# Kernel tuning notes

Measured on AMD Instinct MI355X. Metric: run time of the kernel, lower is better.

## Reference

```python
import jax, jax.numpy as jnp
import numpy as np

N = 50000
E = 1600000
IN_DIM = 128
HEADS = 4
OUT_DIM = 32
NEG_SLOPE = 0.2


def setup_inputs() -> dict:
    key = jax.random.key(0)
    k1, k2, k3, k4, k5, k6 = jax.random.split(key, 6)
    x = jax.random.normal(k1, (N, IN_DIM), dtype=jnp.float32)
    src = jax.random.randint(k2, (E,), 0, N)
    dst = jax.random.randint(k3, (E,), 0, N)
    edge_index = jnp.stack([src, dst], axis=0).astype(jnp.int64)
    W = jax.random.normal(k4, (IN_DIM, HEADS * OUT_DIM), dtype=jnp.float32) * 0.08
    att = jax.random.normal(k5, (HEADS, 2 * OUT_DIM), dtype=jnp.float32) * 0.1
    bias = jnp.zeros((HEADS * OUT_DIM,), dtype=jnp.float32)
    return {"x": x, "edge_index": edge_index, "W": W, "att": att, "bias": bias}


def reference(x, edge_index, W, att, bias):
    src, dst = edge_index[0], edge_index[1]
    n = x.shape[0]
    # Linear projection -> [N, H, F]
    Wh = (x @ W).reshape(n, HEADS, OUT_DIM)
    # Per-node attention score halves (equivalent to (cat[Wh_i,Wh_j]*att).sum(-1))
    a_src = jnp.einsum("nhf,hf->nh", Wh, att[:, :OUT_DIM])  # [N, H]
    a_dst = jnp.einsum("nhf,hf->nh", Wh, att[:, OUT_DIM:])  # [N, H]
    logits = jax.nn.leaky_relu(a_src[src] + a_dst[dst], negative_slope=NEG_SLOPE)  # [E, H]
    # Segment softmax over destination nodes (numerically stable)
    seg_max = jax.ops.segment_max(logits, dst, num_segments=n)  # [N, H]
    exp_s = jnp.exp(logits - seg_max[dst])
    denom = jnp.clip(jax.ops.segment_sum(exp_s, dst, num_segments=n), 1e-9, None)
    alpha = exp_s / denom[dst]  # [E, H]
    # Weighted messages from SOURCE features, scatter-sum to destinations
    messages = alpha[:, :, None] * Wh[src]  # [E, H, F]
    out = jax.ops.segment_sum(messages.reshape(-1, HEADS * OUT_DIM), dst, num_segments=n)
    return out + bias
```

## Files before the change

kernel.cpp:

```cpp
#include <hip/hip_runtime.h>
#include <hip/hip_fp16.h>
#include <math.h>

#define N_NODES 50000
#define E_EDGES 1600000
#define IN_DIM 128
#define HEADS 4
#define OUT_DIM 32
#define HF 128
#define NEG_SLOPE 0.2f
#define NBUCK 196
#define BCAP 8800

typedef _Float16 half8 __attribute__((ext_vector_type(8)));
typedef float float4v __attribute__((ext_vector_type(4)));

__global__ __launch_bounds__(256) void gat_wt(
        const float* __restrict__ W, _Float16* __restrict__ Wt) {
    const int n = blockIdx.x * 2 + (threadIdx.x >> 7);
    const int k = threadIdx.x & 127;
    Wt[n * 128 + k] = (_Float16)W[k * 128 + n];
}

__global__ __launch_bounds__(256) void gat_proj(
        const float* __restrict__ x, const _Float16* __restrict__ Wt,
        const float* __restrict__ att, __half* __restrict__ Whh,
        float* __restrict__ a_src, float* __restrict__ a_dst) {
    __shared__ _Float16 xsh[64][136];
    __shared__ float4 wfrag[2048 / 4 * 8 / 8];
    __shared__ float atts[256];

    const int tid  = threadIdx.x;
    const int lane = tid & 63;
    const int wv   = tid >> 6;
    const int l15  = lane & 15;
    const int quad = lane >> 4;

    if (tid < 64) ((float4*)atts)[tid] = ((const float4*)att)[tid];

    const int rowBase  = blockIdx.x * 64;
    const int rowsHere = min(64, N_NODES - rowBase);

    const float4* x4 = (const float4*)(x + (size_t)rowBase * IN_DIM);
    for (int i = tid; i < rowsHere * 32; i += 256) {
        const int r = i >> 5, q = i & 31;
        float4 v = x4[i];
        _Float16* p = &xsh[r][q * 4];
        p[0] = (_Float16)v.x; p[1] = (_Float16)v.y;
        p[2] = (_Float16)v.z; p[3] = (_Float16)v.w;
    }

    __shared__ float4 wf[32 * 64];
    for (int i = tid; i < 32 * 64; i += 256) {
        const int ln = i & 63, c = i >> 6;
        const int s = c >> 3, t = c & 7;
        const int n = t * 16 + (ln & 15);
        const int k = s * 32 + (ln >> 4) * 8;
        wf[i] = *(const float4*)(Wt + n * 128 + k);
    }
    __syncthreads();

    float4v acc[8] = {};
    half8 afr[4];
#pragma unroll
    for (int s = 0; s < 4; ++s)
        afr[s] = *(const half8*)&xsh[wv * 16 + l15][s * 32 + quad * 8];
#pragma unroll
    for (int s = 0; s < 4; ++s) {
#pragma unroll
        for (int t = 0; t < 8; ++t) {
            half8 b = *(const half8*)&wf[(s * 8 + t) * 64 + lane];
            acc[t] = __builtin_amdgcn_mfma_f32_16x16x32_f16(afr[s], b, acc[t], 0, 0, 0);
        }
    }

    float ps[4][4] = {}, pd[4][4] = {};
#pragma unroll
    for (int t = 0; t < 8; ++t) {
        const int g = t >> 1;
        const int f = ((t & 1) << 4) + l15;
        const float as_ = atts[g * 64 + f];
        const float ad_ = atts[g * 64 + 32 + f];
#pragma unroll
        for (int reg = 0; reg < 4; ++reg) {
            ps[reg][g] = fmaf(acc[t][reg], as_, ps[reg][g]);
            pd[reg][g] = fmaf(acc[t][reg], ad_, pd[reg][g]);
        }
    }
#pragma unroll
    for (int reg = 0; reg < 4; ++reg) {
        const int rloc = wv * 16 + quad * 4 + reg;
        const int row = rowBase + rloc;
        if (rloc < rowsHere) {
#pragma unroll
            for (int t = 0; t < 8; ++t)
                Whh[(size_t)row * HF + t * 16 + l15] = __float2half(acc[t][reg]);
        }
#pragma unroll
        for (int g = 0; g < 4; ++g) {
#pragma unroll
            for (int d = 1; d < 16; d <<= 1) {
                ps[reg][g] += __shfl_xor(ps[reg][g], d, 64);
                pd[reg][g] += __shfl_xor(pd[reg][g], d, 64);
            }
        }
        if (rloc < rowsHere && l15 < 4) {
            a_src[row * HEADS + l15] = ps[reg][l15];
            a_dst[row * HEADS + l15] = pd[reg][l15];
        }
    }
}

__global__ __launch_bounds__(256) void gat_p1(
        const int* __restrict__ ei, int* __restrict__ gCount,
        unsigned int* __restrict__ gBuck) {
    __shared__ int hist[NBUCK];
    __shared__ int cur[NBUCK];
    const int t = threadIdx.x;
    for (int i = t; i < NBUCK; i += 256) hist[i] = 0;
    __syncthreads();

    unsigned int keys[16];
    bool valid[4];
    const int base4 = blockIdx.x * 1024 + t;
#pragma unroll
    for (int j = 0; j < 4; ++j) {
        const int i4 = base4 + 256 * j;
        valid[j] = (i4 < E_EDGES / 4);
        if (valid[j]) {
            const int4 s4 = ((const int4*)ei)[i4];
            const int4 d4 = ((const int4*)(ei + E_EDGES))[i4];
            keys[j * 4 + 0] = ((unsigned)d4.x << 16) | (unsigned)s4.x;
            keys[j * 4 + 1] = ((unsigned)d4.y << 16) | (unsigned)s4.y;
            keys[j * 4 + 2] = ((unsigned)d4.z << 16) | (unsigned)s4.z;
            keys[j * 4 + 3] = ((unsigned)d4.w << 16) | (unsigned)s4.w;
#pragma unroll
            for (int q = 0; q < 4; ++q)
                atomicAdd(&hist[keys[j * 4 + q] >> 24], 1);
        }
    }
    __syncthreads();
    for (int i = t; i < NBUCK; i += 256)
        cur[i] = atomicAdd(&gCount[i], hist[i]);
    __syncthreads();
#pragma unroll
    for (int j = 0; j < 4; ++j) {
        if (!valid[j]) continue;
#pragma unroll
        for (int q = 0; q < 4; ++q) {
            const unsigned int k = keys[j * 4 + q];
            const int b = k >> 24;
            const int p = atomicAdd(&cur[b], 1);
            if (p < BCAP) gBuck[(size_t)b * BCAP + p] = k;
        }
    }
}

__global__ __launch_bounds__(256) void gat_p2(
        const int* __restrict__ gCount, const unsigned int* __restrict__ gBuck,
        unsigned short* __restrict__ csr, int* __restrict__ offsets) {
    __shared__ int pre[256];
    __shared__ int hist[256];
    __shared__ int loc[256];
    __shared__ unsigned short out16[BCAP];
    const int b = blockIdx.x;
    const int t = threadIdx.x;

    int v = (t < NBUCK) ? min(gCount[t], BCAP) : 0;
    pre[t] = v;
    __syncthreads();
#pragma unroll
    for (int d = 1; d < 256; d <<= 1) {
        int u = (t >= d) ? pre[t - d] : 0;
        __syncthreads();
        pre[t] += u;
        __syncthreads();
    }
    const int total = pre[255];
    const int baseb = (b > 0) ? pre[b - 1] : 0;
    const int cnt = min(gCount[b], BCAP);

    hist[t] = 0;
    __syncthreads();
    for (int i = t; i < cnt; i += 256)
        atomicAdd(&hist[(gBuck[(size_t)b * BCAP + i] >> 16) & 255], 1);
    __syncthreads();
    const int hv = hist[t];
    loc[t] = hv;
    __syncthreads();
#pragma unroll
    for (int d = 1; d < 256; d <<= 1) {
        int u = (t >= d) ? loc[t - d] : 0;
        __syncthreads();
        loc[t] += u;
        __syncthreads();
    }
    const int myloc = loc[t] - hv;
    const int node = b * 256 + t;
    if (node < N_NODES) offsets[node] = baseb + myloc;
    if (b == 0 && t == 0) offsets[N_NODES] = total;
    __syncthreads();

    hist[t] = myloc;
    __syncthreads();
    for (int i = t; i < cnt; i += 256) {
        const unsigned int k = gBuck[(size_t)b * BCAP + i];
        const int n = (k >> 16) & 255;
        const int r = atomicAdd(&hist[n], 1);
        out16[r] = (unsigned short)(k & 0xFFFFu);
    }
    __syncthreads();
    for (int i = t; i < cnt; i += 256)
        csr[baseb + i] = out16[i];
}

__global__ __launch_bounds__(256) void gat_gather(
        const int* __restrict__ offsets, const unsigned short* __restrict__ csr,
        const float* __restrict__ a_src, const float* __restrict__ a_dst,
        const __half* __restrict__ Whh, const float* __restrict__ bias,
        float* __restrict__ out) {
    const int node = blockIdx.x * 4 + (threadIdx.x >> 6);
    const int lane = threadIdx.x & 63;
    if (node >= N_NODES) return;
    const int h = lane >> 4;
    const int hbase = lane & 48;
    const int sub = lane & 15;
    const float ad = a_dst[node * HEADS + h];
    const __half2* __restrict__ Wh2 = (const __half2*)Whh;

    float accx = 0.f, accy = 0.f, denOwn = 0.f;
    const int beg = offsets[node];
    const int cnt = offsets[node + 1] - beg;

    for (int base = 0; base < cnt; base += 64) {
        const int rem = min(64, cnt - base);
        const int idx = (base + lane < cnt) ? (int)csr[beg + base + lane] : 0;
        const int nchunk = (rem + 15) >> 4;
        for (int cj = 0; cj < nchunk; ++cj) {
            const int e0 = cj << 4;
            const int sOwn = __shfl(idx, e0 + sub, 64);
            float t = a_src[sOwn * 4 + h] + ad;
            t = fmaxf(t, NEG_SLOPE * t);
            float wOwn = __expf(t);
            if (base + e0 + sub >= cnt) wOwn = 0.f;
            denOwn += wOwn;

            const int jmax = min(16, rem - e0);
            if (jmax == 16) {
                int ss[16];
#pragma unroll
                for (int j = 0; j < 16; ++j) ss[j] = __shfl(idx, e0 + j, 64);
                __half2 vv[16];
#pragma unroll
                for (int j = 0; j < 16; ++j)
                    vv[j] = Wh2[(size_t)ss[j] * 64 + lane];
                float ww[16];
#pragma unroll
                for (int j = 0; j < 16; ++j) ww[j] = __shfl(wOwn, hbase + j, 64);
#pragma unroll
                for (int j = 0; j < 16; ++j) {
                    const float2 f = __half22float2(vv[j]);
                    accx = fmaf(ww[j], f.x, accx);
                    accy = fmaf(ww[j], f.y, accy);
                }
            } else {
                for (int j = 0; j < jmax; ++j) {
                    const int s = __shfl(idx, e0 + j, 64);
                    const float w = __shfl(wOwn, hbase + j, 64);
                    const float2 v = __half22float2(Wh2[(size_t)s * 64 + lane]);
                    accx = fmaf(w, v.x, accx);
                    accy = fmaf(w, v.y, accy);
                }
            }
        }
    }
    float den = denOwn;
    den += __shfl_xor(den, 1, 64);
    den += __shfl_xor(den, 2, 64);
    den += __shfl_xor(den, 4, 64);
    den += __shfl_xor(den, 8, 64);

    const float inv = 1.f / fmaxf(den, 1e-9f);
    const float2 b2 = ((const float2*)bias)[lane];
    float2 o = {accx * inv + b2.x, accy * inv + b2.y};
    ((float2*)out)[(size_t)node * 64 + lane] = o;
}

extern "C" void kernel_launch(void* const* d_in, const int* in_sizes, int n_in,
                              void* d_out, int out_size, void* d_ws, size_t ws_size,
                              hipStream_t stream) {
    const float* x    = (const float*)d_in[0];
    const int*   ei   = (const int*)d_in[1];
    const float* W    = (const float*)d_in[2];
    const float* att  = (const float*)d_in[3];
    const float* bias = (const float*)d_in[4];
    float* out = (float*)d_out;

    __half* Whh   = (__half*)d_ws;
    float* a_src  = (float*)(Whh + (size_t)N_NODES * HF);
    float* a_dst  = a_src + (size_t)N_NODES * HEADS;
    unsigned int* gBuck = (unsigned int*)(a_dst + (size_t)N_NODES * HEADS);
    unsigned short* csr = (unsigned short*)(gBuck + (size_t)NBUCK * BCAP);
    int*   offsets = (int*)(csr + (size_t)E_EDGES);
    int*   gCount  = offsets + N_NODES + 8;
    _Float16* Wt   = (_Float16*)(gCount + 256);

    hipMemsetAsync(gCount, 0, NBUCK * sizeof(int), stream);
    gat_wt<<<64, 256, 0, stream>>>(W, Wt);
    gat_proj<<<(N_NODES + 63) / 64, 256, 0, stream>>>(x, Wt, att, Whh, a_src, a_dst);
    gat_p1<<<(E_EDGES / 4 + 1023) / 1024, 256, 0, stream>>>(ei, gCount, gBuck);
    gat_p2<<<NBUCK, 256, 0, stream>>>(gCount, gBuck, csr, offsets);
    gat_gather<<<(N_NODES + 3) / 4, 256, 0, stream>>>(offsets, csr, a_src,
                                                      a_dst, Whh, bias, out);
}
```

Measured before the change: 211.2 us.

## Fuse projection and edge bucketing into one launch; fold memset into prep

The memset of the bucket counters moves into the W-transpose kernel. The projection and edge-bucketing kernels become a single launch that splits blocks by index, so the two independent stages can run concurrently and two launches are dropped. The gather inner loop replaces the fully unrolled 16-edge path with a 4-way unrolled loop plus a remainder loop. This lowers register pressure but keeps fewer loads in flight. The fused kernel uses a 51 KB shared buffer for all blocks, which may reduce occupancy for the bucketing blocks.

Result: faster. 186.8 us (-11.6%).

```diff
diff --git a/kernel.cpp b/kernel.cpp
--- a/kernel.cpp
+++ b/kernel.cpp
@@ -11,147 +11,151 @@
 #define NEG_SLOPE 0.2f
 #define NBUCK 196
 #define BCAP 8800
+#define PROJ_NB 782
+#define P1_NB 391
 
 typedef _Float16 half8 __attribute__((ext_vector_type(8)));
 typedef float float4v __attribute__((ext_vector_type(4)));
 
-__global__ __launch_bounds__(256) void gat_wt(
-        const float* __restrict__ W, _Float16* __restrict__ Wt) {
+__global__ __launch_bounds__(256) void gat_prep(
+        const float* __restrict__ W, _Float16* __restrict__ Wt,
+        int* __restrict__ gCount) {
+    if (blockIdx.x == 0 && threadIdx.x < NBUCK) gCount[threadIdx.x] = 0;
     const int n = blockIdx.x * 2 + (threadIdx.x >> 7);
     const int k = threadIdx.x & 127;
     Wt[n * 128 + k] = (_Float16)W[k * 128 + n];
 }
 
-__global__ __launch_bounds__(256) void gat_proj(
+__global__ __launch_bounds__(256) void gat_fused(
         const float* __restrict__ x, const _Float16* __restrict__ Wt,
         const float* __restrict__ att, __half* __restrict__ Whh,
-        float* __restrict__ a_src, float* __restrict__ a_dst) {
-    __shared__ _Float16 xsh[64][136];
-    __shared__ float4 wfrag[2048 / 4 * 8 / 8];
-    __shared__ float atts[256];
-
-    const int tid  = threadIdx.x;
-    const int lane = tid & 63;
-    const int wv   = tid >> 6;
-    const int l15  = lane & 15;
-    const int quad = lane >> 4;
-
-    if (tid < 64) ((float4*)atts)[tid] = ((const float4*)att)[tid];
-
-    const int rowBase  = blockIdx.x * 64;
-    const int rowsHere = min(64, N_NODES - rowBase);
-
-    const float4* x4 = (const float4*)(x + (size_t)rowBase * IN_DIM);
-    for (int i = tid; i < rowsHere * 32; i += 256) {
-        const int r = i >> 5, q = i & 31;
-        float4 v = x4[i];
-        _Float16* p = &xsh[r][q * 4];
-        p[0] = (_Float16)v.x; p[1] = (_Float16)v.y;
-        p[2] = (_Float16)v.z; p[3] = (_Float16)v.w;
-    }
-
-    __shared__ float4 wf[32 * 64];
-    for (int i = tid; i < 32 * 64; i += 256) {
-        const int ln = i & 63, c = i >> 6;
-        const int s = c >> 3, t = c & 7;
-        const int n = t * 16 + (ln & 15);
-        const int k = s * 32 + (ln >> 4) * 8;
-        wf[i] = *(const float4*)(Wt + n * 128 + k);
-    }
-    __syncthreads();
-
-    float4v acc[8] = {};
-    half8 afr[4];
-#pragma unroll
-    for (int s = 0; s < 4; ++s)
-        afr[s] = *(const half8*)&xsh[wv * 16 + l15][s * 32 + quad * 8];
-#pragma unroll
-    for (int s = 0; s < 4; ++s) {
-#pragma unroll
-        for (int t = 0; t < 8; ++t) {
-            half8 b = *(const half8*)&wf[(s * 8 + t) * 64 + lane];
-            acc[t] = __builtin_amdgcn_mfma_f32_16x16x32_f16(afr[s], b, acc[t], 0, 0, 0);
-        }
-    }
-
-    float ps[4][4] = {}, pd[4][4] = {};
-#pragma unroll
-    for (int t = 0; t < 8; ++t) {
-        const int g = t >> 1;
-        const int f = ((t & 1) << 4) + l15;
-        const float as_ = atts[g * 64 + f];
-        const float ad_ = atts[g * 64 + 32 + f];
-#pragma unroll
-        for (int reg = 0; reg < 4; ++reg) {
-            ps[reg][g] = fmaf(acc[t][reg], as_, ps[reg][g]);
-            pd[reg][g] = fmaf(acc[t][reg], ad_, pd[reg][g]);
-        }
-    }
-#pragma unroll
-    for (int reg = 0; reg < 4; ++reg) {
-        const int rloc = wv * 16 + quad * 4 + reg;
-        const int row = rowBase + rloc;
-        if (rloc < rowsHere) {
-#pragma unroll
-            for (int t = 0; t < 8; ++t)
-                Whh[(size_t)row * HF + t * 16 + l15] = __float2half(acc[t][reg]);
-        }
-#pragma unroll
-        for (int g = 0; g < 4; ++g) {
-#pragma unroll
-            for (int d = 1; d < 16; d <<= 1) {
-                ps[reg][g] += __shfl_xor(ps[reg][g], d, 64);
-                pd[reg][g] += __shfl_xor(pd[reg][g], d, 64);
-            }
-        }
-        if (rloc < rowsHere && l15 < 4) {
-            a_src[row * HEADS + l15] = ps[reg][l15];
-            a_dst[row * HEADS + l15] = pd[reg][l15];
-        }
-    }
-}
-
-__global__ __launch_bounds__(256) void gat_p1(
+        float* __restrict__ a_src, float* __restrict__ a_dst,
         const int* __restrict__ ei, int* __restrict__ gCount,
         unsigned int* __restrict__ gBuck) {
-    __shared__ int hist[NBUCK];
-    __shared__ int cur[NBUCK];
-    const int t = threadIdx.x;
-    for (int i = t; i < NBUCK; i += 256) hist[i] = 0;
-    __syncthreads();
-
-    unsigned int keys[16];
-    bool valid[4];
-    const int base4 = blockIdx.x * 1024 + t;
-#pragma unroll
-    for (int j = 0; j < 4; ++j) {
-        const int i4 = base4 + 256 * j;
-        valid[j] = (i4 < E_EDGES / 4);
-        if (valid[j]) {
-            const int4 s4 = ((const int4*)ei)[i4];
-            const int4 d4 = ((const int4*)(ei + E_EDGES))[i4];
-            keys[j * 4 + 0] = ((unsigned)d4.x << 16) | (unsigned)s4.x;
-            keys[j * 4 + 1] = ((unsigned)d4.y << 16) | (unsigned)s4.y;
-            keys[j * 4 + 2] = ((unsigned)d4.z << 16) | (unsigned)s4.z;
-            keys[j * 4 + 3] = ((unsigned)d4.w << 16) | (unsigned)s4.w;
-#pragma unroll
-            for (int q = 0; q < 4; ++q)
-                atomicAdd(&hist[keys[j * 4 + q] >> 24], 1);
-        }
-    }
-    __syncthreads();
-    for (int i = t; i < NBUCK; i += 256)
-        cur[i] = atomicAdd(&gCount[i], hist[i]);
-    __syncthreads();
-#pragma unroll
-    for (int j = 0; j < 4; ++j) {
-        if (!valid[j]) continue;
-#pragma unroll
-        for (int q = 0; q < 4; ++q) {
-            const unsigned int k = keys[j * 4 + q];
-            const int b = k >> 24;
-            const int p = atomicAdd(&cur[b], 1);
-            if (p < BCAP) gBuck[(size_t)b * BCAP + p] = k;
+    __shared__ __align__(16) char smem[51200];
+    const int tid = threadIdx.x;
+
+    if (blockIdx.x < PROJ_NB) {
+        _Float16 (*xsh)[136] = (_Float16(*)[136])smem;
+        float4* wf  = (float4*)(smem + 17408);
+        float* atts = (float*)(smem + 17408 + 32768);
+
+        const int lane = tid & 63;
+        const int wv   = tid >> 6;
+        const int l15  = lane & 15;
+        const int quad = lane >> 4;
+
+        if (tid < 64) ((float4*)atts)[tid] = ((const float4*)att)[tid];
+
+        const int rowBase  = blockIdx.x * 64;
+        const int rowsHere = min(64, N_NODES - rowBase);
+
+        const float4* x4 = (const float4*)(x + (size_t)rowBase * IN_DIM);
+        for (int i = tid; i < rowsHere * 32; i += 256) {
+            const int r = i >> 5, q = i & 31;
+            float4 v = x4[i];
+            _Float16* p = &xsh[r][q * 4];
+            p[0] = (_Float16)v.x; p[1] = (_Float16)v.y;
+            p[2] = (_Float16)v.z; p[3] = (_Float16)v.w;
+        }
+        for (int i = tid; i < 32 * 64; i += 256) {
+            const int ln = i & 63, c = i >> 6;
+            const int s = c >> 3, t = c & 7;
+            const int n = t * 16 + (ln & 15);
+            const int k = s * 32 + (ln >> 4) * 8;
+            wf[i] = *(const float4*)(Wt + n * 128 + k);
+        }
+        __syncthreads();
+
+        float4v acc[8] = {};
+        half8 afr[4];
+#pragma unroll
+        for (int s = 0; s < 4; ++s)
+            afr[s] = *(const half8*)&xsh[wv * 16 + l15][s * 32 + quad * 8];
+#pragma unroll
+        for (int s = 0; s < 4; ++s) {
+#pragma unroll
+            for (int t = 0; t < 8; ++t) {
+                half8 b = *(const half8*)&wf[(s * 8 + t) * 64 + lane];
+                acc[t] = __builtin_amdgcn_mfma_f32_16x16x32_f16(afr[s], b, acc[t], 0, 0, 0);
+            }
+        }
+
+        float ps[4][4] = {}, pd[4][4] = {};
+#pragma unroll
+        for (int t = 0; t < 8; ++t) {
+            const int g = t >> 1;
+            const int f = ((t & 1) << 4) + l15;
+            const float as_ = atts[g * 64 + f];
+            const float ad_ = atts[g * 64 + 32 + f];
+#pragma unroll
+            for (int reg = 0; reg < 4; ++reg) {
+                ps[reg][g] = fmaf(acc[t][reg], as_, ps[reg][g]);
+                pd[reg][g] = fmaf(acc[t][reg], ad_, pd[reg][g]);
+            }
+        }
+#pragma unroll
+        for (int reg = 0; reg < 4; ++reg) {
+            const int rloc = wv * 16 + quad * 4 + reg;
+            const int row = rowBase + rloc;
+            if (rloc < rowsHere) {
+#pragma unroll
+                for (int t = 0; t < 8; ++t)
+                    Whh[(size_t)row * HF + t * 16 + l15] = __float2half(acc[t][reg]);
+            }
+#pragma unroll
+            for (int g = 0; g < 4; ++g) {
+#pragma unroll
+                for (int d = 1; d < 16; d <<= 1) {
+                    ps[reg][g] += __shfl_xor(ps[reg][g], d, 64);
+                    pd[reg][g] += __shfl_xor(pd[reg][g], d, 64);
+                }
+            }
+            if (rloc < rowsHere && l15 < 4) {
+                a_src[row * HEADS + l15] = ps[reg][l15];
+                a_dst[row * HEADS + l15] = pd[reg][l15];
+            }
+        }
+    } else {
+        int* hist = (int*)smem;
+        int* cur  = hist + NBUCK;
+        const int bid = blockIdx.x - PROJ_NB;
+        for (int i = tid; i < NBUCK; i += 256) hist[i] = 0;
+        __syncthreads();
+
+        unsigned int keys[16];
+        bool valid[4];
+        const int base4 = bid * 1024 + tid;
+#pragma unroll
+        for (int j = 0; j < 4; ++j) {
+            const int i4 = base4 + 256 * j;
+            valid[j] = (i4 < E_EDGES / 4);
+            if (valid[j]) {
+                const int4 s4 = ((const int4*)ei)[i4];
+                const int4 d4 = ((const int4*)(ei + E_EDGES))[i4];
+                keys[j * 4 + 0] = ((unsigned)d4.x << 16) | (unsigned)s4.x;
+                keys[j * 4 + 1] = ((unsigned)d4.y << 16) | (unsigned)s4.y;
+                keys[j * 4 + 2] = ((unsigned)d4.z << 16) | (unsigned)s4.z;
+                keys[j * 4 + 3] = ((unsigned)d4.w << 16) | (unsigned)s4.w;
+#pragma unroll
+                for (int q = 0; q < 4; ++q)
+                    atomicAdd(&hist[keys[j * 4 + q] >> 24], 1);
+            }
+        }
+        __syncthreads();
+        for (int i = tid; i < NBUCK; i += 256)
+            cur[i] = atomicAdd(&gCount[i], hist[i]);
+        __syncthreads();
+#pragma unroll
+        for (int j = 0; j < 4; ++j) {
+            if (!valid[j]) continue;
+#pragma unroll
+            for (int q = 0; q < 4; ++q) {
+                const unsigned int k = keys[j * 4 + q];
+                const int b = k >> 24;
+                const int p = atomicAdd(&cur[b], 1);
+                if (p < BCAP) gBuck[(size_t)b * BCAP + p] = k;
+            }
         }
     }
 }
@@ -246,31 +250,35 @@
             denOwn += wOwn;
 
             const int jmax = min(16, rem - e0);
-            if (jmax == 16) {
-                int ss[16];
-#pragma unroll
-                for (int j = 0; j < 16; ++j) ss[j] = __shfl(idx, e0 + j, 64);
-                __half2 vv[16];
-#pragma unroll
-                for (int j = 0; j < 16; ++j)
-                    vv[j] = Wh2[(size_t)ss[j] * 64 + lane];
-                float ww[16];
-#pragma unroll
-                for (int j = 0; j < 16; ++j) ww[j] = __shfl(wOwn, hbase + j, 64);
-#pragma unroll
-                for (int j = 0; j < 16; ++j) {
-                    const float2 f = __half22float2(vv[j]);
-                    accx = fmaf(ww[j], f.x, accx);
-                    accy = fmaf(ww[j], f.y, accy);
-                }
-            } else {
-                for (int j = 0; j < jmax; ++j) {
-                    const int s = __shfl(idx, e0 + j, 64);
-                    const float w = __shfl(wOwn, hbase + j, 64);
-                    const float2 v = __half22float2(Wh2[(size_t)s * 64 + lane]);
-                    accx = fmaf(w, v.x, accx);
-                    accy = fmaf(w, v.y, accy);
-                }
+            int j = 0;
+            for (; j + 4 <= jmax; j += 4) {
+                const int s0 = __shfl(idx, e0 + j,     64);
+                const int s1 = __shfl(idx, e0 + j + 1, 64);
+                const int s2 = __shfl(idx, e0 + j + 2, 64);
+                const int s3 = __shfl(idx, e0 + j + 3, 64);
+                const __half2 v0 = Wh2[(size_t)s0 * 64 + lane];
+                const __half2 v1 = Wh2[(size_t)s1 * 64 + lane];
+                const __half2 v2 = Wh2[(size_t)s2 * 64 + lane];
+                const __half2 v3 = Wh2[(size_t)s3 * 64 + lane];
+                const float w0 = __shfl(wOwn, hbase + j,     64);
+                const float w1 = __shfl(wOwn, hbase + j + 1, 64);
+                const float w2 = __shfl(wOwn, hbase + j + 2, 64);
+                const float w3 = __shfl(wOwn, hbase + j + 3, 64);
+                const float2 f0 = __half22float2(v0);
+                const float2 f1 = __half22float2(v1);
+                const float2 f2 = __half22float2(v2);
+                const float2 f3 = __half22float2(v3);
+                accx = fmaf(w0, f0.x, accx); accy = fmaf(w0, f0.y, accy);
+                accx = fmaf(w1, f1.x, accx); accy = fmaf(w1, f1.y, accy);
+                accx = fmaf(w2, f2.x, accx); accy = fmaf(w2, f2.y, accy);
+                accx = fmaf(w3, f3.x, accx); accy = fmaf(w3, f3.y, accy);
+            }
+            for (; j < jmax; ++j) {
+                const int s = __shfl(idx, e0 + j, 64);
+                const float w = __shfl(wOwn, hbase + j, 64);
+                const float2 v = __half22float2(Wh2[(size_t)s * 64 + lane]);
+                accx = fmaf(w, v.x, accx);
+                accy = fmaf(w, v.y, accy);
             }
         }
     }
@@ -305,10 +313,9 @@
     int*   gCount  = offsets + N_NODES + 8;
     _Float16* Wt   = (_Float16*)(gCount + 256);
 
-    hipMemsetAsync(gCount, 0, NBUCK * sizeof(int), stream);
-    gat_wt<<<64, 256, 0, stream>>>(W, Wt);
-    gat_proj<<<(N_NODES + 63) / 64, 256, 0, stream>>>(x, Wt, att, Whh, a_src, a_dst);
-    gat_p1<<<(E_EDGES / 4 + 1023) / 1024, 256, 0, stream>>>(ei, gCount, gBuck);
+    gat_prep<<<64, 256, 0, stream>>>(W, Wt, gCount);
+    gat_fused<<<PROJ_NB + P1_NB, 256, 0, stream>>>(x, Wt, att, Whh, a_src,
+                                                   a_dst, ei, gCount, gBuck);
     gat_p2<<<NBUCK, 256, 0, stream>>>(gCount, gBuck, csr, offsets);
     gat_gather<<<(N_NODES + 3) / 4, 256, 0, stream>>>(offsets, csr, a_src,
                                                       a_dst, Whh, bias, out);
```
